# Kernel tuning notes

Measured on AMD Instinct MI355X. Metric: run time of the kernel, lower is better.

The kernel has to match this reference:

```python
import jax, jax.numpy as jnp
import numpy as np

B, N, IN_DIM, OUT_DIM = 8, 2048, 128, 128


def setup_inputs() -> dict:
    key = jax.random.key(0)
    k_a, k_h, k_wp, k_bp, k_wa, k_ba = jax.random.split(key, 6)
    a = jax.random.uniform(k_a, (B, N, N), dtype=jnp.float32)
    h = jax.random.normal(k_h, (B, N, IN_DIM), dtype=jnp.float32)
    # nn.Linear(in_dim, out_dim): y = x @ W^T + b ; store W already transposed.
    W_proj = jax.random.normal(k_wp, (IN_DIM, OUT_DIM), dtype=jnp.float32) / np.sqrt(IN_DIM)
    b_proj = jax.random.normal(k_bp, (OUT_DIM,), dtype=jnp.float32) * 0.01
    # nn.Linear(2*out_dim, 1): weight vector of length 2*out_dim + scalar bias.
    w_att = jax.random.normal(k_wa, (2 * OUT_DIM,), dtype=jnp.float32) / np.sqrt(2 * OUT_DIM)
    b_att = jax.random.normal(k_ba, (), dtype=jnp.float32) * 0.01
    return {"a": a, "h": h, "W_proj": W_proj, "b_proj": b_proj,
            "w_att": w_att, "b_att": b_att}


def reference(a, h, W_proj, b_proj, w_att, b_att):
    # h: [B, N, in_dim] -> [B, N, out_dim]
    h = h @ W_proj + b_proj
    d = w_att.shape[0] // 2
    # GAT decomposition: attention(cat(h_i, h_j)) = h_i.w_src + h_j.w_dst + b
    # (identical math to expand+cat+Linear, without the O(B*N^2*2D) tensor)
    s = h @ w_att[:d]            # [B, N] contribution of row node i
    t = h @ w_att[d:]            # [B, N] contribution of col node j
    e = jax.nn.relu(s[:, :, None] + t[:, None, :] + b_att)  # [B, N, N]
    att = jnp.exp(e) * a
    att = att / jnp.sum(att, axis=-1, keepdims=True)
    return att @ h + h           # [B, N, out_dim]
```

## Files before the change

### kernel.cpp

```cpp
#include <hip/hip_runtime.h>
#include <hip/hip_bf16.h>

#define NB 8
#define NN 2048
#define DD 128
#define NT 32

typedef __attribute__((ext_vector_type(8))) short short8v;
typedef __attribute__((ext_vector_type(4))) float f32x4;

__device__ __forceinline__ unsigned short f2bf(float x) {
    unsigned int u = __float_as_uint(x);
    u += 0x7FFFu + ((u >> 16) & 1u);
    return (unsigned short)(u >> 16);
}

__global__ __launch_bounds__(256) void proj_kernel(
    const float* __restrict__ h, const float* __restrict__ W,
    const float* __restrict__ bias, const float* __restrict__ watt,
    float* __restrict__ hp, unsigned short* __restrict__ hpT,
    float* __restrict__ s, float* __restrict__ t)
{
    __shared__ float Ws[64][132];
    __shared__ float hs[64][68];
    const int tid = threadIdx.x;
    const int rowbase = blockIdx.x * 64;
    const int rg = tid >> 3;
    const int dg = tid & 7;

    const float4* W4 = (const float4*)W;
    const float4* h4 = (const float4*)h;

    float acc[2][16];
    #pragma unroll
    for (int r = 0; r < 2; ++r)
        #pragma unroll
        for (int d = 0; d < 16; ++d) acc[r][d] = 0.f;

    for (int p = 0; p < 2; ++p) {
        #pragma unroll
        for (int q = 0; q < 8; ++q) {
            int f = tid + 256 * q;
            float4 v = W4[2048 * p + f];
            *(float4*)&Ws[f >> 5][4 * (f & 31)] = v;
        }
        #pragma unroll
        for (int q = 0; q < 4; ++q) {
            int f = tid + 256 * q;
            int r = f >> 4, c4 = f & 15;
            float4 v = h4[(size_t)(rowbase + r) * 32 + 16 * p + c4];
            *(float4*)&hs[r][4 * c4] = v;
        }
        __syncthreads();

        #pragma unroll 8
        for (int k = 0; k < 64; ++k) {
            float h0 = hs[2 * rg][k];
            float h1 = hs[2 * rg + 1][k];
            float4 w0 = *(const float4*)&Ws[k][dg * 16];
            float4 w1 = *(const float4*)&Ws[k][dg * 16 + 4];
            float4 w2 = *(const float4*)&Ws[k][dg * 16 + 8];
            float4 w3 = *(const float4*)&Ws[k][dg * 16 + 12];
            float wv[16] = {w0.x,w0.y,w0.z,w0.w, w1.x,w1.y,w1.z,w1.w,
                            w2.x,w2.y,w2.z,w2.w, w3.x,w3.y,w3.z,w3.w};
            #pragma unroll
            for (int d = 0; d < 16; ++d) {
                acc[0][d] += h0 * wv[d];
                acc[1][d] += h1 * wv[d];
            }
        }
        __syncthreads();
    }

    const float4* b4 = (const float4*)bias;
    #pragma unroll
    for (int dq = 0; dq < 4; ++dq) {
        float4 bv = b4[dg * 4 + dq];
        #pragma unroll
        for (int r = 0; r < 2; ++r) {
            acc[r][4 * dq + 0] += bv.x;
            acc[r][4 * dq + 1] += bv.y;
            acc[r][4 * dq + 2] += bv.z;
            acc[r][4 * dq + 3] += bv.w;
        }
    }
    #pragma unroll
    for (int r = 0; r < 2; ++r) {
        float4* o = (float4*)(hp + (size_t)(rowbase + 2 * rg + r) * 128);
        #pragma unroll
        for (int dq = 0; dq < 4; ++dq) {
            float4 v = {acc[r][4*dq+0], acc[r][4*dq+1], acc[r][4*dq+2], acc[r][4*dq+3]};
            o[dg * 4 + dq] = v;
        }
    }
    {
        int rowpair = ((rowbase & (NN - 1)) >> 1) + rg;
        int bb = rowbase >> 11;
        unsigned int* hT32 = (unsigned int*)hpT;
        #pragma unroll
        for (int dd = 0; dd < 16; ++dd) {
            int d = dg * 16 + dd;
            unsigned int pk = (unsigned int)f2bf(acc[0][dd]) |
                              ((unsigned int)f2bf(acc[1][dd]) << 16);
            hT32[(((size_t)bb * 128 + d) << 10) + rowpair] = pk;
        }
    }
    const float4* w4 = (const float4*)watt;
    float sp[2] = {0.f, 0.f}, tp[2] = {0.f, 0.f};
    #pragma unroll
    for (int q = 0; q < 4; ++q) {
        float4 wsa = w4[dg * 4 + q];
        float4 wta = w4[32 + dg * 4 + q];
        #pragma unroll
        for (int r = 0; r < 2; ++r) {
            sp[r] += acc[r][4*q+0]*wsa.x + acc[r][4*q+1]*wsa.y
                   + acc[r][4*q+2]*wsa.z + acc[r][4*q+3]*wsa.w;
            tp[r] += acc[r][4*q+0]*wta.x + acc[r][4*q+1]*wta.y
                   + acc[r][4*q+2]*wta.z + acc[r][4*q+3]*wta.w;
        }
    }
    #pragma unroll
    for (int r = 0; r < 2; ++r) {
        float v = sp[r], u = tp[r];
        v += __shfl_xor(v, 1, 64); u += __shfl_xor(u, 1, 64);
        v += __shfl_xor(v, 2, 64); u += __shfl_xor(u, 2, 64);
        v += __shfl_xor(v, 4, 64); u += __shfl_xor(u, 4, 64);
        if (dg == 0) {
            s[rowbase + 2 * rg + r] = v;
            t[rowbase + 2 * rg + r] = u;
        }
    }
}

__global__ __launch_bounds__(256, 4) void fused_kernel(
    const float* __restrict__ a, const float* __restrict__ hp,
    const unsigned short* __restrict__ hpT,
    const float* __restrict__ s, const float* __restrict__ t,
    const float* __restrict__ battp, float* __restrict__ out)
{
    __shared__ unsigned short hpT_s[2][128 * 64];
    __shared__ unsigned short w_s[2][16 * 64];
    __shared__ float wsum_s[16];

    const int tid  = threadIdx.x;
    const int lane = tid & 63;
    const int wv   = tid >> 6;
    const int b     = blockIdx.x >> 7;
    const int ibase = (blockIdx.x & 127) * 16;
    const int bN    = b * NN;

    const int rowA = tid >> 4;
    const int q    = tid & 15;
    const int sd   = tid >> 1;
    const int sj   = (tid & 1) * 64;

    const float batt = battp[0];
    const float4* a4 = (const float4*)a;
    const float4* t4 = (const float4*)t;
    const float s_reg = s[bN + ibase + rowA];
    const size_t arow = (size_t)(bN + ibase + rowA) * 512;
    const unsigned short* hTg = hpT + (((size_t)(b * 128 + sd)) << 11) + (tid & 1) * 32;

    float wsum_p = 0.f;
    f32x4 acc0 = {0.f, 0.f, 0.f, 0.f};
    f32x4 acc1 = {0.f, 0.f, 0.f, 0.f};

    float4 a_nx, t_nx;
    uint4 hv0, hv1, hv2, hv3;

#define LOADA(tt) do { \
        a_nx = a4[arow + (tt) * 16 + q]; \
        t_nx = t4[(bN >> 2) + (tt) * 16 + q]; \
    } while (0)

#define STAGELOAD(tt) do { \
        const unsigned short* gp = hTg + (tt) * 64; \
        hv0 = *(const uint4*)(gp);      hv1 = *(const uint4*)(gp + 8); \
        hv2 = *(const uint4*)(gp + 16); hv3 = *(const uint4*)(gp + 24); \
    } while (0)

#define STAGEWRITE(nb) do { \
        char* lb = (char*)hpT_s[nb]; \
        int swz = (sd & 7) << 4; \
        int bo = (sd << 7) + sj; \
        *(uint4*)(lb + ((bo     ) ^ swz)) = hv0; \
        *(uint4*)(lb + ((bo + 16) ^ swz)) = hv1; \
        *(uint4*)(lb + ((bo + 32) ^ swz)) = hv2; \
        *(uint4*)(lb + ((bo + 48) ^ swz)) = hv3; \
    } while (0)

#define PHASEA(nb) do { \
        float p0 = __expf(fmaxf(s_reg + t_nx.x + batt, 0.f)) * a_nx.x; \
        float p1 = __expf(fmaxf(s_reg + t_nx.y + batt, 0.f)) * a_nx.y; \
        float p2 = __expf(fmaxf(s_reg + t_nx.z + batt, 0.f)) * a_nx.z; \
        float p3 = __expf(fmaxf(s_reg + t_nx.w + batt, 0.f)) * a_nx.w; \
        wsum_p += (p0 + p1) + (p2 + p3); \
        unsigned int u0 = (unsigned int)f2bf(p0) | ((unsigned int)f2bf(p1) << 16); \
        unsigned int u1 = (unsigned int)f2bf(p2) | ((unsigned int)f2bf(p3) << 16); \
        uint2 uu; uu.x = u0; uu.y = u1; \
        *(uint2*)((char*)w_s[nb] + (((rowA << 7) + (q << 3)) ^ ((rowA & 7) << 4))) = uu; \
    } while (0)

#define DOMFMA(cb) do { \
        const char* wb = (const char*)w_s[cb]; \
        const char* hb = (const char*)hpT_s[cb]; \
        int r = lane & 15; \
        int kb = (lane >> 4) << 4; \
        int swz = (r & 7) << 4; \
        short8v A0 = *(const short8v*)(wb + (((r << 7) + kb     ) ^ swz)); \
        short8v A1 = *(const short8v*)(wb + (((r << 7) + kb + 64) ^ swz)); \
        int d0 = (wv << 5) + r; \
        short8v B00 = *(const short8v*)(hb + (((d0 << 7) + kb     ) ^ swz)); \
        short8v B01 = *(const short8v*)(hb + (((d0 << 7) + kb + 64) ^ swz)); \
        short8v B10 = *(const short8v*)(hb + ((((d0 + 16) << 7) + kb     ) ^ swz)); \
        short8v B11 = *(const short8v*)(hb + ((((d0 + 16) << 7) + kb + 64) ^ swz)); \
        acc0 = __builtin_amdgcn_mfma_f32_16x16x32_bf16(A0, B00, acc0, 0, 0, 0); \
        acc1 = __builtin_amdgcn_mfma_f32_16x16x32_bf16(A0, B10, acc1, 0, 0, 0); \
        acc0 = __builtin_amdgcn_mfma_f32_16x16x32_bf16(A1, B01, acc0, 0, 0, 0); \
        acc1 = __builtin_amdgcn_mfma_f32_16x16x32_bf16(A1, B11, acc1, 0, 0, 0); \
    } while (0)

    LOADA(0);
    STAGELOAD(0);
    PHASEA(0);
    STAGEWRITE(0);
    __syncthreads();

    int cur = 0;
    #pragma unroll 2
    for (int tt = 0; tt < NT; ++tt) {
        if (tt < NT - 1) { LOADA(tt + 1); STAGELOAD(tt + 1); }
        DOMFMA(cur);
        if (tt < NT - 1) { PHASEA(cur ^ 1); STAGEWRITE(cur ^ 1); }
        __syncthreads();
        cur ^= 1;
    }

    {
        float v = wsum_p;
        v += __shfl_xor(v, 1, 64);
        v += __shfl_xor(v, 2, 64);
        v += __shfl_xor(v, 4, 64);
        v += __shfl_xor(v, 8, 64);
        if (q == 0) wsum_s[rowA] = v;
    }
    __syncthreads();

    {
        int r = lane & 15;
        int rloc = (lane >> 4) << 2;
        float inv0 = 1.0f / wsum_s[rloc + 0];
        float inv1 = 1.0f / wsum_s[rloc + 1];
        float inv2 = 1.0f / wsum_s[rloc + 2];
        float inv3 = 1.0f / wsum_s[rloc + 3];
        int d0 = (wv << 5) + r;
        const float* hpb = hp + (size_t)(bN + ibase) * 128;
        float* ob = out + (size_t)(bN + ibase) * 128;
        ob[(rloc + 0) * 128 + d0]      = acc0.x * inv0 + hpb[(rloc + 0) * 128 + d0];
        ob[(rloc + 1) * 128 + d0]      = acc0.y * inv1 + hpb[(rloc + 1) * 128 + d0];
        ob[(rloc + 2) * 128 + d0]      = acc0.z * inv2 + hpb[(rloc + 2) * 128 + d0];
        ob[(rloc + 3) * 128 + d0]      = acc0.w * inv3 + hpb[(rloc + 3) * 128 + d0];
        ob[(rloc + 0) * 128 + d0 + 16] = acc1.x * inv0 + hpb[(rloc + 0) * 128 + d0 + 16];
        ob[(rloc + 1) * 128 + d0 + 16] = acc1.y * inv1 + hpb[(rloc + 1) * 128 + d0 + 16];
        ob[(rloc + 2) * 128 + d0 + 16] = acc1.z * inv2 + hpb[(rloc + 2) * 128 + d0 + 16];
        ob[(rloc + 3) * 128 + d0 + 16] = acc1.w * inv3 + hpb[(rloc + 3) * 128 + d0 + 16];
    }
#undef LOADA
#undef STAGELOAD
#undef STAGEWRITE
#undef PHASEA
#undef DOMFMA
}

extern "C" void kernel_launch(void* const* d_in, const int* in_sizes, int n_in,
                              void* d_out, int out_size, void* d_ws, size_t ws_size,
                              hipStream_t stream) {
    const float* a      = (const float*)d_in[0];
    const float* h      = (const float*)d_in[1];
    const float* W_proj = (const float*)d_in[2];
    const float* b_proj = (const float*)d_in[3];
    const float* w_att  = (const float*)d_in[4];
    const float* b_att  = (const float*)d_in[5];
    float* out = (float*)d_out;

    float* hp = (float*)d_ws;
    float* s  = hp + (size_t)NB * NN * DD;
    float* t  = s + (size_t)NB * NN;
    unsigned short* hpT = (unsigned short*)(t + (size_t)NB * NN);

    proj_kernel<<<256, 256, 0, stream>>>(h, W_proj, b_proj, w_att, hp, hpT, s, t);
    fused_kernel<<<1024, 256, 0, stream>>>(a, hp, hpT, s, t, b_att, out);
}
```

Measured before the change: 264.3 us.

## Load MFMA B operands directly from global into registers, drop LDS staging

The bf16 transposed projection tile is no longer staged through shared memory. Each lane now loads its MFMA B fragments straight from global memory into registers, and the pipeline is restructured as a two-deep register double buffer with attention weights and h prefetched one or two tiles ahead. This removes LDS traffic and the 32 KB shared buffer, which may allow higher occupancy. In exchange it adds register pressure, and global B loads of only 16 bytes per lane may reduce coalescing and rely on L2 hits, since all 128 blocks of a batch read the same data.

Result: faster. 257.6 us (-2.5%).

```diff
diff --git a/kernel.cpp b/kernel.cpp
--- a/kernel.cpp
+++ b/kernel.cpp
@@ -138,7 +138,6 @@
     const float* __restrict__ s, const float* __restrict__ t,
     const float* __restrict__ battp, float* __restrict__ out)
 {
-    __shared__ unsigned short hpT_s[2][128 * 64];
     __shared__ unsigned short w_s[2][16 * 64];
     __shared__ float wsum_s[16];
 
@@ -151,89 +150,79 @@
 
     const int rowA = tid >> 4;
     const int q    = tid & 15;
-    const int sd   = tid >> 1;
-    const int sj   = (tid & 1) * 64;
+
+    const int r  = lane & 15;
+    const int kg = lane >> 4;
+    const int d0 = (wv << 5) + r;
 
     const float batt = battp[0];
     const float4* a4 = (const float4*)a;
     const float4* t4 = (const float4*)t;
     const float s_reg = s[bN + ibase + rowA];
     const size_t arow = (size_t)(bN + ibase + rowA) * 512;
-    const unsigned short* hTg = hpT + (((size_t)(b * 128 + sd)) << 11) + (tid & 1) * 32;
+
+    const unsigned short* pB0 = hpT + (((size_t)(b * 128 + d0)) << 11) + (kg << 3);
+    const unsigned short* pB1 = pB0 + ((size_t)16 << 11);
 
     float wsum_p = 0.f;
     f32x4 acc0 = {0.f, 0.f, 0.f, 0.f};
     f32x4 acc1 = {0.f, 0.f, 0.f, 0.f};
 
-    float4 a_nx, t_nx;
-    uint4 hv0, hv1, hv2, hv3;
-
-#define LOADA(tt) do { \
-        a_nx = a4[arow + (tt) * 16 + q]; \
-        t_nx = t4[(bN >> 2) + (tt) * 16 + q]; \
-    } while (0)
-
-#define STAGELOAD(tt) do { \
-        const unsigned short* gp = hTg + (tt) * 64; \
-        hv0 = *(const uint4*)(gp);      hv1 = *(const uint4*)(gp + 8); \
-        hv2 = *(const uint4*)(gp + 16); hv3 = *(const uint4*)(gp + 24); \
-    } while (0)
-
-#define STAGEWRITE(nb) do { \
-        char* lb = (char*)hpT_s[nb]; \
-        int swz = (sd & 7) << 4; \
-        int bo = (sd << 7) + sj; \
-        *(uint4*)(lb + ((bo     ) ^ swz)) = hv0; \
-        *(uint4*)(lb + ((bo + 16) ^ swz)) = hv1; \
-        *(uint4*)(lb + ((bo + 32) ^ swz)) = hv2; \
-        *(uint4*)(lb + ((bo + 48) ^ swz)) = hv3; \
-    } while (0)
-
-#define PHASEA(nb) do { \
-        float p0 = __expf(fmaxf(s_reg + t_nx.x + batt, 0.f)) * a_nx.x; \
-        float p1 = __expf(fmaxf(s_reg + t_nx.y + batt, 0.f)) * a_nx.y; \
-        float p2 = __expf(fmaxf(s_reg + t_nx.z + batt, 0.f)) * a_nx.z; \
-        float p3 = __expf(fmaxf(s_reg + t_nx.w + batt, 0.f)) * a_nx.w; \
+    float4 av[2], tv[2];
+    short8v B00[2], B01[2], B10[2], B11[2];
+
+#define LOADAT(P, k) do { \
+        av[P] = a4[arow + (k) * 16 + q]; \
+        tv[P] = t4[(bN >> 2) + (k) * 16 + q]; \
+    } while (0)
+
+#define LOADB(P, k) do { \
+        const short8v* b0 = (const short8v*)(pB0 + (k) * 64); \
+        const short8v* b1 = (const short8v*)(pB1 + (k) * 64); \
+        B00[P] = b0[0]; B01[P] = b0[4]; \
+        B10[P] = b1[0]; B11[P] = b1[4]; \
+    } while (0)
+
+#define PHASEA(P) do { \
+        float p0 = __expf(fmaxf(s_reg + tv[P].x + batt, 0.f)) * av[P].x; \
+        float p1 = __expf(fmaxf(s_reg + tv[P].y + batt, 0.f)) * av[P].y; \
+        float p2 = __expf(fmaxf(s_reg + tv[P].z + batt, 0.f)) * av[P].z; \
+        float p3 = __expf(fmaxf(s_reg + tv[P].w + batt, 0.f)) * av[P].w; \
         wsum_p += (p0 + p1) + (p2 + p3); \
         unsigned int u0 = (unsigned int)f2bf(p0) | ((unsigned int)f2bf(p1) << 16); \
         unsigned int u1 = (unsigned int)f2bf(p2) | ((unsigned int)f2bf(p3) << 16); \
         uint2 uu; uu.x = u0; uu.y = u1; \
-        *(uint2*)((char*)w_s[nb] + (((rowA << 7) + (q << 3)) ^ ((rowA & 7) << 4))) = uu; \
-    } while (0)
-
-#define DOMFMA(cb) do { \
-        const char* wb = (const char*)w_s[cb]; \
-        const char* hb = (const char*)hpT_s[cb]; \
-        int r = lane & 15; \
-        int kb = (lane >> 4) << 4; \
+        *(uint2*)((char*)w_s[P] + (((rowA << 7) + (q << 3)) ^ ((rowA & 7) << 4))) = uu; \
+    } while (0)
+
+#define DOMFMA(P) do { \
+        const char* wb = (const char*)w_s[P]; \
+        int kbB = kg << 4; \
         int swz = (r & 7) << 4; \
-        short8v A0 = *(const short8v*)(wb + (((r << 7) + kb     ) ^ swz)); \
-        short8v A1 = *(const short8v*)(wb + (((r << 7) + kb + 64) ^ swz)); \
-        int d0 = (wv << 5) + r; \
-        short8v B00 = *(const short8v*)(hb + (((d0 << 7) + kb     ) ^ swz)); \
-        short8v B01 = *(const short8v*)(hb + (((d0 << 7) + kb + 64) ^ swz)); \
-        short8v B10 = *(const short8v*)(hb + ((((d0 + 16) << 7) + kb     ) ^ swz)); \
-        short8v B11 = *(const short8v*)(hb + ((((d0 + 16) << 7) + kb + 64) ^ swz)); \
-        acc0 = __builtin_amdgcn_mfma_f32_16x16x32_bf16(A0, B00, acc0, 0, 0, 0); \
-        acc1 = __builtin_amdgcn_mfma_f32_16x16x32_bf16(A0, B10, acc1, 0, 0, 0); \
-        acc0 = __builtin_amdgcn_mfma_f32_16x16x32_bf16(A1, B01, acc0, 0, 0, 0); \
-        acc1 = __builtin_amdgcn_mfma_f32_16x16x32_bf16(A1, B11, acc1, 0, 0, 0); \
-    } while (0)
-
-    LOADA(0);
-    STAGELOAD(0);
+        short8v A0 = *(const short8v*)(wb + (((r << 7) + kbB     ) ^ swz)); \
+        short8v A1 = *(const short8v*)(wb + (((r << 7) + kbB + 64) ^ swz)); \
+        acc0 = __builtin_amdgcn_mfma_f32_16x16x32_bf16(A0, B00[P], acc0, 0, 0, 0); \
+        acc1 = __builtin_amdgcn_mfma_f32_16x16x32_bf16(A0, B10[P], acc1, 0, 0, 0); \
+        acc0 = __builtin_amdgcn_mfma_f32_16x16x32_bf16(A1, B01[P], acc0, 0, 0, 0); \
+        acc1 = __builtin_amdgcn_mfma_f32_16x16x32_bf16(A1, B11[P], acc1, 0, 0, 0); \
+    } while (0)
+
+    LOADAT(0, 0); LOADB(0, 0);
+    LOADAT(1, 1); LOADB(1, 1);
     PHASEA(0);
-    STAGEWRITE(0);
     __syncthreads();
 
-    int cur = 0;
-    #pragma unroll 2
-    for (int tt = 0; tt < NT; ++tt) {
-        if (tt < NT - 1) { LOADA(tt + 1); STAGELOAD(tt + 1); }
-        DOMFMA(cur);
-        if (tt < NT - 1) { PHASEA(cur ^ 1); STAGEWRITE(cur ^ 1); }
-        __syncthreads();
-        cur ^= 1;
+    for (int tt = 0; tt < NT; tt += 2) {
+        PHASEA(1);
+        if (tt + 2 < NT) LOADAT(0, tt + 2);
+        DOMFMA(0);
+        if (tt + 2 < NT) LOADB(0, tt + 2);
+        __syncthreads();
+        if (tt + 2 < NT) PHASEA(0);
+        if (tt + 3 < NT) LOADAT(1, tt + 3);
+        DOMFMA(1);
+        if (tt + 3 < NT) LOADB(1, tt + 3);
+        __syncthreads();
     }
 
     {
@@ -247,13 +236,11 @@
     __syncthreads();
 
     {
-        int r = lane & 15;
         int rloc = (lane >> 4) << 2;
         float inv0 = 1.0f / wsum_s[rloc + 0];
         float inv1 = 1.0f / wsum_s[rloc + 1];
         float inv2 = 1.0f / wsum_s[rloc + 2];
         float inv3 = 1.0f / wsum_s[rloc + 3];
-        int d0 = (wv << 5) + r;
         const float* hpb = hp + (size_t)(bN + ibase) * 128;
         float* ob = out + (size_t)(bN + ibase) * 128;
         ob[(rloc + 0) * 128 + d0]      = acc0.x * inv0 + hpb[(rloc + 0) * 128 + d0];
@@ -265,9 +252,8 @@
         ob[(rloc + 2) * 128 + d0 + 16] = acc1.z * inv2 + hpb[(rloc + 2) * 128 + d0 + 16];
         ob[(rloc + 3) * 128 + d0 + 16] = acc1.w * inv3 + hpb[(rloc + 3) * 128 + d0 + 16];
     }
-#undef LOADA
-#undef STAGELOAD
-#undef STAGEWRITE
+#undef LOADAT
+#undef LOADB
 #undef PHASEA
 #undef DOMFMA
 }
```
